# Kernel tuning notes

Hardware: AMD Instinct MI355X
Metric: run time of the kernel (lower is better)

## Reference

```python
import jax, jax.numpy as jnp
import numpy as np

B, T, K, D = 512, 2048, 8, 32
DT = 0.05  # dt0 in the original diffrax Euler solve


def setup_inputs() -> dict:
    key = jax.random.key(0)
    ks = jax.random.split(key, 6)
    z0 = jax.random.normal(ks[0], (B, D), dtype=jnp.float32)
    # per-step unnormalized state probabilities s(t) (jnp.average divides by their sum)
    s_probs = jax.random.uniform(ks[1], (T, B, K), dtype=jnp.float32) + 1e-3
    # standard-normal increments; dW = sqrt(dt) * noise (Euler-Maruyama Brownian step)
    noise = jax.random.normal(ks[2], (T, B, D), dtype=jnp.float32)
    # parameters, initialized exactly as in SwitchableDrift / SwitchableDiffusion
    A_s = jax.random.normal(ks[3], (K, D, D), dtype=jnp.float32) * 0.1 - jnp.eye(D, dtype=jnp.float32) * 0.5
    b_s = jax.random.normal(ks[4], (K, D), dtype=jnp.float32) * 0.1
    Q_chol = jax.random.uniform(ks[5], (K, D), dtype=jnp.float32) * 0.1 + 0.1
    return {"z0": z0, "s_probs": s_probs, "noise": noise, "A_s": A_s, "b_s": b_s, "Q_chol": Q_chol}


def reference(z0, s_probs, noise, A_s, b_s, Q_chol):
    """Euler-Maruyama integration of the switching linear SDE:
       dz = E_s[A_s z + b_s] dt + diag(E_s[Q_s]) dW.
       Expectations are probability-weighted averages (jnp.average semantics).
       Returns ys with shape [T, B, D] (states after each step)."""
    dW = jnp.sqrt(jnp.asarray(DT, z0.dtype)) * noise  # [T, B, D]

    def step(z, inp):
        w, dw = inp                                    # w: [B,K], dw: [B,D]
        wsum = jnp.sum(w, axis=-1, keepdims=True)      # jnp.average normalizer
        # expected drift: (sum_k w_k (A_k z + b_k)) / sum_k w_k
        drift = (jnp.einsum('bk,kij,bj->bi', w, A_s, z) + w @ b_s) / wsum
        # expected diagonal diffusion: (sum_k w_k Q_k) / sum_k w_k
        diff = (w @ Q_chol) / wsum                     # [B,D] diagonal of g
        z_new = z + DT * drift + diff * dw             # diag(g) @ dW == diff * dw
        return z_new, z_new

    _, ys = jax.lax.scan(step, z0, (s_probs, dW))
    return ys
```

## Files before the change

kernel.cpp:

```cpp
#include <hip/hip_runtime.h>
#include <stdint.h>

#define NBATCH 512
#define NT     2048
#define NK     8
#define ND     32
#define PF     4

typedef float f2 __attribute__((ext_vector_type(2)));
typedef unsigned int u2 __attribute__((ext_vector_type(2)));

__device__ __forceinline__ float halfsum(float x) {
#if defined(__has_builtin) && __has_builtin(__builtin_amdgcn_permlane32_swap)
    u2 r = __builtin_amdgcn_permlane32_swap(__float_as_uint(x), __float_as_uint(x),
                                            false, false);
    return __uint_as_float(r.x) + __uint_as_float(r.y);
#else
    return x + __shfl_xor(x, 32);
#endif
}

__global__ __launch_bounds__(64, 1) void slds_kernel(
    const float* __restrict__ z0,
    const float* __restrict__ s_probs,
    const float* __restrict__ noise,
    const float* __restrict__ A_s,
    const float* __restrict__ b_s,
    const float* __restrict__ Q_chol,
    float* __restrict__ ys)
{
    const int b    = blockIdx.x;
    const int lane = threadIdx.x;
    const int i    = lane & 31;
    const int kh   = lane >> 5;

    const float dt  = 0.05f;
    const float sdt = 0.22360679774997896f;

    f2 a2[4][16];
#pragma unroll
    for (int kk = 0; kk < 4; ++kk) {
        const float4* ap = (const float4*)(A_s + (((size_t)(kh * 4 + kk) * ND + i) * ND));
#pragma unroll
        for (int q = 0; q < 8; ++q) {
            float4 v = ap[q];
            a2[kk][q * 2 + 0] = f2{v.x, v.y};
            a2[kk][q * 2 + 1] = f2{v.z, v.w};
        }
    }
    float breg[4], qreg[4];
#pragma unroll
    for (int kk = 0; kk < 4; ++kk) {
        breg[kk] = b_s[(kh * 4 + kk) * ND + i];
        qreg[kk] = Q_chol[(kh * 4 + kk) * ND + i];
    }

    float zi = z0[b * ND + i];
    f2 z2[16];
#pragma unroll
    for (int j = 0; j < 16; ++j) {
        z2[j].x = __int_as_float(__builtin_amdgcn_readlane(__float_as_int(zi), 2 * j));
        z2[j].y = __int_as_float(__builtin_amdgcn_readlane(__float_as_int(zi), 2 * j + 1));
    }

    const float4* wbase = (const float4*)s_probs;
    const float*  nbase = noise;

    float4 wv[PF];
    float  nr[PF];
#pragma unroll
    for (int u = 0; u < PF; ++u) {
        const size_t o = (size_t)u * (NBATCH * 2) + (size_t)b * 2 + kh;
        wv[u] = wbase[o];
        nr[u] = nbase[((size_t)u * NBATCH + b) * ND + i];
    }

    for (int t = 0; t < NT; t += PF) {
#pragma unroll
        for (int u = 0; u < PF; ++u) {
            const int tt = t + u;
            const float4 wa  = wv[u];
            const float  nrc = nr[u];

            int tp = tt + PF; if (tp > NT - 1) tp = NT - 1;
            const size_t op = (size_t)tp * (NBATCH * 2) + (size_t)b * 2 + kh;
            wv[u] = wbase[op];
            nr[u] = nbase[((size_t)tp * NBATCH + b) * ND + i];

            const float w0 = wa.x, w1 = wa.y, w2 = wa.z, w3 = wa.w;
            float psum = (w0 + w1) + (w2 + w3);
            float wsum = halfsum(psum);
            float inv  = __builtin_amdgcn_rcpf(wsum);
            float g    = sdt * nrc;

            float acc = 0.f, qacc = 0.f;
#pragma unroll
            for (int kk = 0; kk < 4; ++kk) {
                f2 y01 = f2{breg[kk], 0.f};
#pragma unroll
                for (int j = 0; j < 16; ++j)
                    y01 = __builtin_elementwise_fma(a2[kk][j], z2[j], y01);
                const float wk = (kk == 0) ? w0 : (kk == 1) ? w1 : (kk == 2) ? w2 : w3;
                acc  = fmaf(wk, y01.x + y01.y, acc);
                qacc = fmaf(wk, qreg[kk], qacc);
            }

            acc  = halfsum(acc);
            qacc = halfsum(qacc);

            float znew = fmaf(inv, fmaf(dt, acc, g * qacc), zi);

            const size_t oofs = ((size_t)tt * NBATCH + b) * ND + i;
            if (lane < 32) {
                __builtin_nontemporal_store(znew, &ys[oofs]);
            }

#pragma unroll
            for (int j = 0; j < 16; ++j) {
                z2[j].x = __int_as_float(__builtin_amdgcn_readlane(__float_as_int(znew), 2 * j));
                z2[j].y = __int_as_float(__builtin_amdgcn_readlane(__float_as_int(znew), 2 * j + 1));
            }
            zi = znew;
        }
    }
}

extern "C" void kernel_launch(void* const* d_in, const int* in_sizes, int n_in,
                              void* d_out, int out_size, void* d_ws, size_t ws_size,
                              hipStream_t stream) {
    const float* z0 = (const float*)d_in[0];
    const float* sp = (const float*)d_in[1];
    const float* no = (const float*)d_in[2];
    const float* As = (const float*)d_in[3];
    const float* bs = (const float*)d_in[4];
    const float* Qc = (const float*)d_in[5];
    float* ys = (float*)d_out;

    slds_kernel<<<dim3(NBATCH), dim3(64), 0, stream>>>(z0, sp, no, As, bs, Qc, ys);
}
```

Before: 961.1 us.

## Split per-batch switch-mode matvecs across four waves with LDS reduction

Each block now runs four waves instead of one, with each lane handling a single mode k rather than four. This cuts the serial FMA chain per timestep by roughly four times. Partial drift and diffusion sums are combined through a double-buffered shared array with one __syncthreads per step. The cost is a block-wide barrier and LDS round trip on the latency-bound recurrence, plus redundant loads and readlanes in every wave.

```diff
diff --git a/kernel.cpp b/kernel.cpp
--- a/kernel.cpp
+++ b/kernel.cpp
@@ -20,7 +20,7 @@
 #endif
 }
 
-__global__ __launch_bounds__(64, 1) void slds_kernel(
+__global__ __launch_bounds__(256, 1) void slds_kernel(
     const float* __restrict__ z0,
     const float* __restrict__ s_probs,
     const float* __restrict__ noise,
@@ -30,30 +30,30 @@
     float* __restrict__ ys)
 {
     const int b    = blockIdx.x;
-    const int lane = threadIdx.x;
+    const int tid  = threadIdx.x;
+    const int lane = tid & 63;
+    const int w    = tid >> 6;
     const int i    = lane & 31;
-    const int kh   = lane >> 5;
+    const int kp   = lane >> 5;
+    const int k    = w + 4 * kp;
 
     const float dt  = 0.05f;
     const float sdt = 0.22360679774997896f;
 
-    f2 a2[4][16];
-#pragma unroll
-    for (int kk = 0; kk < 4; ++kk) {
-        const float4* ap = (const float4*)(A_s + (((size_t)(kh * 4 + kk) * ND + i) * ND));
+    __shared__ f2 red[2][4][ND];
+
+    f2 a2[16];
+    {
+        const float4* ap = (const float4*)(A_s + ((size_t)k * ND + i) * ND);
 #pragma unroll
         for (int q = 0; q < 8; ++q) {
             float4 v = ap[q];
-            a2[kk][q * 2 + 0] = f2{v.x, v.y};
-            a2[kk][q * 2 + 1] = f2{v.z, v.w};
+            a2[q * 2 + 0] = f2{v.x, v.y};
+            a2[q * 2 + 1] = f2{v.z, v.w};
         }
     }
-    float breg[4], qreg[4];
-#pragma unroll
-    for (int kk = 0; kk < 4; ++kk) {
-        breg[kk] = b_s[(kh * 4 + kk) * ND + i];
-        qreg[kk] = Q_chol[(kh * 4 + kk) * ND + i];
-    }
+    const float breg = b_s[k * ND + i];
+    const float qreg = Q_chol[k * ND + i];
 
     float zi = z0[b * ND + i];
     f2 z2[16];
@@ -70,7 +70,7 @@
     float  nr[PF];
 #pragma unroll
     for (int u = 0; u < PF; ++u) {
-        const size_t o = (size_t)u * (NBATCH * 2) + (size_t)b * 2 + kh;
+        const size_t o = (size_t)u * (NBATCH * 2) + (size_t)b * 2 + kp;
         wv[u] = wbase[o];
         nr[u] = nbase[((size_t)u * NBATCH + b) * ND + i];
     }
@@ -79,39 +79,44 @@
 #pragma unroll
         for (int u = 0; u < PF; ++u) {
             const int tt = t + u;
+            const int p  = tt & 1;
             const float4 wa  = wv[u];
             const float  nrc = nr[u];
 
             int tp = tt + PF; if (tp > NT - 1) tp = NT - 1;
-            const size_t op = (size_t)tp * (NBATCH * 2) + (size_t)b * 2 + kh;
+            const size_t op = (size_t)tp * (NBATCH * 2) + (size_t)b * 2 + kp;
             wv[u] = wbase[op];
             nr[u] = nbase[((size_t)tp * NBATCH + b) * ND + i];
 
-            const float w0 = wa.x, w1 = wa.y, w2 = wa.z, w3 = wa.w;
-            float psum = (w0 + w1) + (w2 + w3);
+            float psum = (wa.x + wa.y) + (wa.z + wa.w);
             float wsum = halfsum(psum);
             float inv  = __builtin_amdgcn_rcpf(wsum);
             float g    = sdt * nrc;
 
-            float acc = 0.f, qacc = 0.f;
+            const float wk = (w == 0) ? wa.x : (w == 1) ? wa.y
+                           : (w == 2) ? wa.z : wa.w;
+
+            f2 y01 = f2{breg, 0.f};
 #pragma unroll
-            for (int kk = 0; kk < 4; ++kk) {
-                f2 y01 = f2{breg[kk], 0.f};
-#pragma unroll
-                for (int j = 0; j < 16; ++j)
-                    y01 = __builtin_elementwise_fma(a2[kk][j], z2[j], y01);
-                const float wk = (kk == 0) ? w0 : (kk == 1) ? w1 : (kk == 2) ? w2 : w3;
-                acc  = fmaf(wk, y01.x + y01.y, acc);
-                qacc = fmaf(wk, qreg[kk], qacc);
-            }
+            for (int j = 0; j < 16; ++j)
+                y01 = __builtin_elementwise_fma(a2[j], z2[j], y01);
+            float pa = wk * (y01.x + y01.y);
+            float pq = wk * qreg;
 
-            acc  = halfsum(acc);
-            qacc = halfsum(qacc);
+            pa = halfsum(pa);
+            pq = halfsum(pq);
+
+            if (lane < 32) red[p][w][i] = f2{pa, pq};
+            __syncthreads();
+            f2 s0 = red[p][0][i], s1 = red[p][1][i];
+            f2 s2 = red[p][2][i], s3 = red[p][3][i];
+            float acc  = (s0.x + s1.x) + (s2.x + s3.x);
+            float qacc = (s0.y + s1.y) + (s2.y + s3.y);
 
             float znew = fmaf(inv, fmaf(dt, acc, g * qacc), zi);
 
-            const size_t oofs = ((size_t)tt * NBATCH + b) * ND + i;
-            if (lane < 32) {
+            if (tid < 32) {
+                const size_t oofs = ((size_t)tt * NBATCH + b) * ND + i;
                 __builtin_nontemporal_store(znew, &ys[oofs]);
             }
 
@@ -136,5 +141,5 @@
     const float* Qc = (const float*)d_in[5];
     float* ys = (float*)d_out;
 
-    slds_kernel<<<dim3(NBATCH), dim3(64), 0, stream>>>(z0, sp, no, As, bs, Qc, ys);
+    slds_kernel<<<dim3(NBATCH), dim3(256), 0, stream>>>(z0, sp, no, As, bs, Qc, ys);
 }
```

Measured after the change: 1.023 ms. 6.5% more time.
